# Kernel tuning notes

Hardware: AMD Instinct MI355X
Metric: run time of the kernel (lower is better)

Reference implementation:

```python
import jax, jax.numpy as jnp
import numpy as np

EPS = 1e-5
NUM_HEADS = 16


def activation_quant(x):
    # 8-bit activation quant with straight-through estimator
    scale = 127.0 / jnp.clip(jnp.max(jnp.abs(x), axis=-1, keepdims=True), 1e-5, None)
    y = jnp.clip(jnp.round(x * scale), -128.0, 127.0) / scale
    return x + jax.lax.stop_gradient(y - x)


def weight_quant(w):
    # ternary {-1,0,1} weight quant with STE
    scale = 1.0 / jnp.clip(jnp.mean(jnp.abs(w)), 1e-5, None)
    wq = jnp.clip(jnp.round(w * scale), -1.0, 1.0) / scale
    return w + jax.lax.stop_gradient(wq - w)


def bitlinear(x, w):
    # F.layer_norm(x, x.shape[1:]): normalize over ALL dims except batch, no affine
    axes = tuple(range(1, x.ndim))
    mu = jnp.mean(x, axis=axes, keepdims=True)
    var = jnp.var(x, axis=axes, keepdims=True)
    xn = (x - mu) * jax.lax.rsqrt(var + EPS)
    return jnp.einsum('bnd,od->bno', activation_quant(xn), weight_quant(w))


def layer_norm(x, gamma, beta):
    mu = jnp.mean(x, axis=-1, keepdims=True)
    var = jnp.var(x, axis=-1, keepdims=True)
    return (x - mu) * jax.lax.rsqrt(var + EPS) * gamma + beta


def setup_inputs() -> dict:
    key = jax.random.key(0)
    k0, k1, k2 = jax.random.split(key, 3)
    B, N, D = 2, 2048, 1024
    return {
        't': jnp.zeros((1,), jnp.float32),
        'x': jax.random.normal(k0, (B, N, D), jnp.float32),
        'w_qkv': jax.random.normal(k1, (3 * D, D), jnp.float32) * 0.02,
        'w_out': jax.random.normal(k2, (D, D), jnp.float32) * 0.02,
        'gamma': jnp.ones((D,), jnp.float32),
        'beta': jnp.zeros((D,), jnp.float32),
    }


def reference(t, x, w_qkv, w_out, gamma, beta):
    B, N, D = x.shape
    H = NUM_HEADS
    hd = D // H
    scale = hd ** -0.5
    h = layer_norm(x, gamma, beta)                     # [B,N,D]
    qkv = bitlinear(h, w_qkv).reshape(B, N, 3, H, hd)   # [B,N,3,H,hd]
    qkv = jnp.transpose(qkv, (2, 0, 3, 1, 4))           # [3,B,H,N,hd]
    q, k, v = qkv[0], qkv[1], qkv[2]
    attn = jax.nn.softmax(jnp.einsum('bhnd,bhmd->bhnm', q, k) * scale, axis=-1)
    out = jnp.einsum('bhnm,bhmd->bhnd', attn, v)        # [B,H,N,hd]
    out = jnp.transpose(out, (0, 2, 1, 3)).reshape(B, N, D)
    return bitlinear(out, w_out)
```

## Files before the change

### kernel.cpp

```cpp
#include <hip/hip_runtime.h>
#include <hip/hip_bf16.h>
#include <hip/hip_fp16.h>
#include <math.h>

typedef __hip_bfloat16 bf16;
typedef int   i32x4  __attribute__((ext_vector_type(4)));
typedef float f32x4  __attribute__((ext_vector_type(4)));
typedef float f32x16 __attribute__((ext_vector_type(16)));
typedef short bfx8   __attribute__((ext_vector_type(8)));

#define EPSV 1e-5f
#define NROWS 4096
#define DIM   1024
#define NSEQ  2048

__device__ __forceinline__ float fexp2(float x){ return __builtin_amdgcn_exp2f(x); }

__device__ __forceinline__ float ldv(const void* p, size_t i, int dt){
  if (dt == 0) return ((const float*)p)[i];
  if (dt == 1) return __bfloat162float(((const bf16*)p)[i]);
  return __half2float(((const __half*)p)[i]);
}
__device__ __forceinline__ float b2f(unsigned u){
  return __uint_as_float(u << 16);
}
__device__ __forceinline__ unsigned short f2bu(float f){
  bf16 t = __float2bfloat16(f);
  return *reinterpret_cast<unsigned short*>(&t);
}

__device__ __forceinline__ void detect(const void* c0, const void* c1,
                                       int& dt, const void*& g, const void*& bta){
  unsigned u0 = *(const unsigned*)c0;
  int gfirst = (u0 != 0u) ? 1 : 0;
  g   = gfirst ? c0 : c1;
  bta = gfirst ? c1 : c0;
  unsigned short g0 = *(const unsigned short*)g;
  dt = (g0 == 0x3F80) ? 1 : ((g0 == 0x3C00) ? 2 : 0);
}

__device__ __forceinline__ float blk_sum(float v, float* sm){
  #pragma unroll
  for (int o = 32; o > 0; o >>= 1) v += __shfl_xor(v, o, 64);
  __syncthreads();
  if ((threadIdx.x & 63) == 0) sm[threadIdx.x >> 6] = v;
  __syncthreads();
  return sm[0] + sm[1] + sm[2] + sm[3];
}
__device__ __forceinline__ double blk_sum_d(double v, double* sm){
  #pragma unroll
  for (int o = 32; o > 0; o >>= 1) v += __shfl_xor(v, o, 64);
  __syncthreads();
  if ((threadIdx.x & 63) == 0) sm[threadIdx.x >> 6] = v;
  __syncthreads();
  return sm[0] + sm[1] + sm[2] + sm[3];
}
__device__ __forceinline__ float blk_max(float v, float* sm){
  #pragma unroll
  for (int o = 32; o > 0; o >>= 1) v = fmaxf(v, __shfl_xor(v, o, 64));
  __syncthreads();
  if ((threadIdx.x & 63) == 0) sm[threadIdx.x >> 6] = v;
  __syncthreads();
  return fmaxf(fmaxf(sm[0], sm[1]), fmaxf(sm[2], sm[3]));
}

__global__ __launch_bounds__(256) void ln_rows(const void* __restrict__ x,
                                               const void* __restrict__ c0,
                                               const void* __restrict__ c1,
                                               unsigned short* __restrict__ h,
                                               double* __restrict__ lnp){
  __shared__ float sm[4];
  __shared__ double smd[4];
  int dt; const void *g, *bta;
  detect(c0, c1, dt, g, bta);
  int row = blockIdx.x;
  int tid = threadIdx.x;
  float v[4]; float s = 0.f;
  float gmv[4], btv[4];
  if (dt == 0){
    float4 v4 = ((const float4*)x)[(size_t)row*256 + tid];
    v[0]=v4.x; v[1]=v4.y; v[2]=v4.z; v[3]=v4.w;
    float4 gm4 = ((const float4*)g)[tid];
    float4 bt4 = ((const float4*)bta)[tid];
    gmv[0]=gm4.x; gmv[1]=gm4.y; gmv[2]=gm4.z; gmv[3]=gm4.w;
    btv[0]=bt4.x; btv[1]=bt4.y; btv[2]=bt4.z; btv[3]=bt4.w;
  } else {
    size_t base = (size_t)row * DIM;
    #pragma unroll
    for (int i = 0; i < 4; ++i){
      v[i]   = ldv(x, base + 4*tid + i, dt);
      gmv[i] = ldv(g, 4*tid + i, dt);
      btv[i] = ldv(bta, 4*tid + i, dt);
    }
  }
  #pragma unroll
  for (int i = 0; i < 4; ++i) s += v[i];
  s = blk_sum(s, sm);
  float mu = s * (1.f/1024.f);
  float d2 = 0.f;
  #pragma unroll
  for (int i = 0; i < 4; ++i){ float d = v[i] - mu; d2 += d*d; }
  d2 = blk_sum(d2, sm);
  float rs = rsqrtf(d2 * (1.f/1024.f) + EPSV);
  float hv[4];
  #pragma unroll
  for (int i = 0; i < 4; ++i) hv[i] = (v[i]-mu)*rs*gmv[i] + btv[i];
  unsigned p0 = (unsigned)f2bu(hv[0]) | ((unsigned)f2bu(hv[1]) << 16);
  unsigned p1 = (unsigned)f2bu(hv[2]) | ((unsigned)f2bu(hv[3]) << 16);
  ((uint2*)h)[(size_t)row*256 + tid] = make_uint2(p0, p1);
  double hs = 0.0, hq = 0.0;
  #pragma unroll
  for (int i = 0; i < 4; ++i){ hs += (double)hv[i]; hq += (double)hv[i]*(double)hv[i]; }
  hs = blk_sum_d(hs, smd);
  hq = blk_sum_d(hq, smd);
  if (tid == 0){ lnp[2*row] = hs; lnp[2*row + 1] = hq; }
}

__global__ __launch_bounds__(256) void abs_reduce_both(const void* __restrict__ wq,
                                                       const void* __restrict__ wo,
                                                       double* __restrict__ awp1,
                                                       double* __restrict__ awp2,
                                                       const void* __restrict__ c0,
                                                       const void* __restrict__ c1){
  __shared__ double smd[4];
  int dt; const void *g, *bta;
  detect(c0, c1, dt, g, bta);
  int blk = blockIdx.x;
  const void* w; int n; int nblk; int bi; double* part;
  if (blk < 512){ w = wq; n = 3*DIM*DIM; nblk = 512; bi = blk;      part = awp1; }
  else          { w = wo; n = DIM*DIM;   nblk = 128; bi = blk - 512; part = awp2; }
  double s = 0.0;
  if (dt == 0){
    const float4* w4 = (const float4*)w;
    int n4 = n >> 2;
    for (int i = bi*256 + threadIdx.x; i < n4; i += nblk*256){
      float4 v = w4[i];
      s += (double)(fabsf(v.x) + fabsf(v.y)) + (double)(fabsf(v.z) + fabsf(v.w));
    }
  } else {
    for (int i = bi*256 + threadIdx.x; i < n; i += nblk*256)
      s += (double)fabsf(ldv(w, i, dt));
  }
  s = blk_sum_d(s, smd);
  if (threadIdx.x == 0) part[bi] = s;
}

__global__ __launch_bounds__(256) void finalize1(float* acc,
                                                 const double* __restrict__ lnp,
                                                 const double* __restrict__ awp1,
                                                 const double* __restrict__ awp2){
  __shared__ double smd[4];
  int tid = threadIdx.x;
  double s0=0, q0=0, s1=0, q1=0, a1=0, a2=0;
  for (int i = tid; i < 2048; i += 256){
    s0 += lnp[2*i];          q0 += lnp[2*i + 1];
    s1 += lnp[2*(i+2048)];   q1 += lnp[2*(i+2048) + 1];
  }
  for (int i = tid; i < 512; i += 256) a1 += awp1[i];
  if (tid < 128) a2 = awp2[tid];
  s0 = blk_sum_d(s0, smd);  q0 = blk_sum_d(q0, smd);
  s1 = blk_sum_d(s1, smd);  q1 = blk_sum_d(q1, smd);
  a1 = blk_sum_d(a1, smd);  a2 = blk_sum_d(a2, smd);
  if (tid == 0){
    const double cnt = 2097152.0;
    double mu0 = s0/cnt, var0 = q0/cnt - mu0*mu0;
    double mu1 = s1/cnt, var1 = q1/cnt - mu1*mu1;
    acc[16] = (float)mu0; acc[17] = (float)(1.0 / sqrt(var0 + 1e-5));
    acc[18] = (float)mu1; acc[19] = (float)(1.0 / sqrt(var1 + 1e-5));
    acc[20] = (float)(1.0 / fmax(a1 / (3.0*1024.0*1024.0), 1e-5));
    acc[21] = (float)(1.0 / fmax(a2 / (1024.0*1024.0), 1e-5));
  }
}

__global__ __launch_bounds__(256) void finalize2(float* acc,
                                                 const double* __restrict__ atp){
  __shared__ double smd[4];
  int tid = threadIdx.x;
  double s0=0, q0=0, s1=0, q1=0;
  for (int i = tid; i < 512; i += 256){
    s0 += atp[2*i];          q0 += atp[2*i + 1];
    s1 += atp[2*(i+512)];    q1 += atp[2*(i+512) + 1];
  }
  s0 = blk_sum_d(s0, smd);  q0 = blk_sum_d(q0, smd);
  s1 = blk_sum_d(s1, smd);  q1 = blk_sum_d(q1, smd);
  if (tid == 0){
    const double cnt = 2097152.0;
    double mu0 = s0/cnt, var0 = q0/cnt - mu0*mu0;
    double mu1 = s1/cnt, var1 = q1/cnt - mu1*mu1;
    acc[22] = (float)mu0; acc[23] = (float)(1.0 / sqrt(var0 + 1e-5));
    acc[24] = (float)mu1; acc[25] = (float)(1.0 / sqrt(var1 + 1e-5));
  }
}

__global__ __launch_bounds__(256) void act_quant_i8b(const unsigned short* __restrict__ buf,
                                                     signed char* __restrict__ qout,
                                                     float* __restrict__ rscale,
                                                     const float* __restrict__ acc,
                                                     int statOff){
  __shared__ float sm[4];
  int row = blockIdx.x;
  int b = row >> 11;
  float mu = acc[statOff + 2*b], rs = acc[statOff + 2*b + 1];
  int tid = threadIdx.x;
  uint2 pk2 = ((const uint2*)buf)[(size_t)row*256 + tid];
  float v[4];
  v[0] = (b2f(pk2.x & 0xffffu) - mu) * rs;
  v[1] = (b2f(pk2.x >> 16)     - mu) * rs;
  v[2] = (b2f(pk2.y & 0xffffu) - mu) * rs;
  v[3] = (b2f(pk2.y >> 16)     - mu) * rs;
  float am = fmaxf(fmaxf(fabsf(v[0]), fabsf(v[1])), fmaxf(fabsf(v[2]), fabsf(v[3])));
  am = blk_max(am, sm);
  am = fmaxf(am, 1e-5f);
  float s127 = 127.f / am;
  unsigned pk = 0;
  #pragma unroll
  for (int i = 0; i < 4; ++i){
    float q = rintf(v[i] * s127);
    q = fminf(fmaxf(q, -128.f), 127.f);
    pk |= ((unsigned)(unsigned char)(signed char)q) << (8*i);
  }
  ((unsigned*)qout)[(size_t)row*256 + tid] = pk;
  if (tid == 0) rscale[row] = am * (1.f/127.f);
}

__global__ __launch_bounds__(256) void w_quant_both(const void* __restrict__ wqv,
                                                    const void* __restrict__ wov,
                                                    signed char* __restrict__ wqk,
                                                    signed char* __restrict__ wqo,
                                                    const float* __restrict__ acc,
                                                    const void* __restrict__ c0,
                                                    const void* __restrict__ c1){
  int dt; const void *g, *bta;
  detect(c0, c1, dt, g, bta);
  const int NQ4 = 786432;
  const int NT4 = 1048576;
  float s1 = acc[20], s2 = acc[21];
  if (dt == 0){
    for (int i = blockIdx.x*256 + threadIdx.x; i < NT4; i += gridDim.x*256){
      int inq = (i < NQ4);
      const float4* src = inq ? (const float4*)wqv : (const float4*)wov;
      unsigned* dst = inq ? (unsigned*)wqk : (unsigned*)wqo;
      int idx = inq ? i : (i - NQ4);
      float scale = inq ? s1 : s2;
      float4 v = src[idx];
      float vv[4] = {v.x, v.y, v.z, v.w};
      unsigned pk = 0;
      #pragma unroll
      for (int j = 0; j < 4; ++j){
        float q = rintf(vv[j] * scale);
        q = fminf(fmaxf(q, -1.f), 1.f);
        pk |= ((unsigned)(unsigned char)(signed char)q) << (8*j);
      }
      dst[idx] = pk;
    }
  } else {
    const int NQ = 3*DIM*DIM, NT = 4*DIM*DIM;
    for (int i = blockIdx.x*256 + threadIdx.x; i < NT; i += gridDim.x*256){
      int inq = (i < NQ);
      int idx = inq ? i : (i - NQ);
      float scale = inq ? s1 : s2;
      float q = rintf(ldv(inq ? wqv : wov, idx, dt) * scale);
      q = fminf(fmaxf(q, -1.f), 1.f);
      (inq ? wqk : wqo)[idx] = (signed char)q;
    }
  }
}

__global__ __launch_bounds__(256) void gemm_i8(const signed char* __restrict__ A,
                                               const signed char* __restrict__ W,
                                               const float* __restrict__ rscale,
                                               const float* __restrict__ acc, int sidx,
                                               float* __restrict__ Cf,
                                               bf16* __restrict__ Cb,
                                               int ldc, int writeBf, float q_prescale){
  __shared__ __attribute__((aligned(16))) signed char Asl[128][80];
  __shared__ __attribute__((aligned(16))) signed char Bsl[128][80];
  int tid = threadIdx.x, lane = tid & 63, w = tid >> 6;
  int wr = w >> 1, wc = w & 1;

  int nwgx = gridDim.x;
  int flat = blockIdx.y * nwgx + blockIdx.x;
  int nwg  = nwgx * gridDim.y;
  int cpx  = nwg >> 3;
  int swz  = (flat & 7) * cpx + (flat >> 3);
  int r0 = (swz / nwgx) * 128, o0 = (swz % nwgx) * 128;

  i32x4 zz = {0,0,0,0};
  i32x4 accv[4][4];
  #pragma unroll
  for (int m = 0; m < 4; ++m)
    #pragma unroll
    for (int n = 0; n < 4; ++n) accv[m][n] = zz;

  int sr0 = tid >> 2, sr1 = sr0 + 64;
  int sc  = (tid & 3) * 16;

  i32x4 a0, a1, b0, b1;
  a0 = *(const i32x4*)(A + (size_t)(r0 + sr0)*1024 + sc);
  a1 = *(const i32x4*)(A + (size_t)(r0 + sr1)*1024 + sc);
  b0 = *(const i32x4*)(W + (size_t)(o0 + sr0)*1024 + sc);
  b1 = *(const i32x4*)(W + (size_t)(o0 + sr1)*1024 + sc);

  for (int k0 = 0; k0 < 1024; k0 += 64){
    __syncthreads();
    *(i32x4*)&Asl[sr0][sc] = a0;
    *(i32x4*)&Asl[sr1][sc] = a1;
    *(i32x4*)&Bsl[sr0][sc] = b0;
    *(i32x4*)&Bsl[sr1][sc] = b1;
    __syncthreads();
    if (k0 + 64 < 1024){
      int kn = k0 + 64;
      a0 = *(const i32x4*)(A + (size_t)(r0 + sr0)*1024 + kn + sc);
      a1 = *(const i32x4*)(A + (size_t)(r0 + sr1)*1024 + kn + sc);
      b0 = *(const i32x4*)(W + (size_t)(o0 + sr0)*1024 + kn + sc);
      b1 = *(const i32x4*)(W + (size_t)(o0 + sr1)*1024 + kn + sc);
    }
    i32x4 af[4], bfr[4];
    #pragma unroll
    for (int m = 0; m < 4; ++m)
      af[m] = *(const i32x4*)&Asl[wr*64 + m*16 + (lane & 15)][(lane >> 4) * 16];
    #pragma unroll
    for (int n = 0; n < 4; ++n)
      bfr[n] = *(const i32x4*)&Bsl[wc*64 + n*16 + (lane & 15)][(lane >> 4) * 16];
    __builtin_amdgcn_s_setprio(1);
    #pragma unroll
    for (int m = 0; m < 4; ++m)
      #pragma unroll
      for (int n = 0; n < 4; ++n)
        accv[m][n] = __builtin_amdgcn_mfma_i32_16x16x64_i8(af[m], bfr[n], accv[m][n], 0, 0, 0);
    __builtin_amdgcn_s_setprio(0);
  }

  float wsc = acc[sidx];
  float cs = (o0 < 1024) ? q_prescale : 1.0f;
  float rf[4][4];
  #pragma unroll
  for (int m = 0; m < 4; ++m)
    #pragma unroll
    for (int r = 0; r < 4; ++r)
      rf[m][r] = rscale[r0 + wr*64 + m*16 + ((lane >> 4) << 2) + r] / wsc * cs;

  #pragma unroll
  for (int m = 0; m < 4; ++m)
    #pragma unroll
    for (int n = 0; n < 4; ++n)
      #pragma unroll
      for (int r = 0; r < 4; ++r){
        float val = (float)accv[m][n][r] * rf[m][r];
        size_t row = (size_t)(r0 + wr*64 + m*16 + ((lane >> 4) << 2) + r);
        int col = o0 + wc*64 + n*16 + (lane & 15);
        if (writeBf) Cb[row * ldc + col] = __float2bfloat16(val);
        else         Cf[row * ldc + col] = val;
      }
}

__global__ __launch_bounds__(128) void attn_mfma(const bf16* __restrict__ qkv,
                                                 unsigned short* __restrict__ out,
                                                 double* __restrict__ atp){
  __shared__ __attribute__((aligned(16))) unsigned short K_lds[64][64];
  __shared__ __attribute__((aligned(16))) unsigned short Vt_lds[64][64];
  __shared__ double smd[2];

  int tid = threadIdx.x, lane = tid & 63, w = tid >> 6;
  int l31 = lane & 31, hi = lane >> 5;

  int flat = blockIdx.y * 32 + blockIdx.x;
  int slot = flat & 7, idx = flat >> 3;
  int bh = slot * 4 + (idx >> 5);
  int qx = idx & 31;
  int b = bh >> 4, h = bh & 15;
  int n0 = qx * 64;
  const unsigned short* qg = (const unsigned short*)qkv;

  char* kB = (char*)K_lds;
  char* vB = (char*)Vt_lds;

  int qrow = b*NSEQ + n0 + w*32 + l31;
  bfx8 qf[4];
  #pragma unroll
  for (int kk = 0; kk < 4; ++kk)
    qf[kk] = *(const bfx8*)(qg + (size_t)qrow*3072 + h*64 + kk*16 + hi*8);

  float m_run = -INFINITY, l_run = 0.f;
  f32x16 acco[2];
  #pragma unroll
  for (int n = 0; n < 2; ++n)
    #pragma unroll
    for (int r = 0; r < 16; ++r) acco[n][r] = 0.f;

  int krow = tid & 63;
  int r2 = tid & 31, dw = tid >> 5;
  int k7 = krow & 7;
  int q7 = l31 & 7;

  bfx8 kc[4], vv[4];
  auto LOADT = [&](int kt){
    size_t kvb = (size_t)(b*NSEQ + kt*64);
    #pragma unroll
    for (int j = 0; j < 4; ++j)
      kc[j] = *(const bfx8*)(qg + (kvb + krow)*3072 + 1024 + h*64 + (w + 2*j)*8);
    vv[0] = *(const bfx8*)(qg + (kvb + 2*r2    )*3072 + 2048 + h*64 + dw*8);
    vv[1] = *(const bfx8*)(qg + (kvb + 2*r2 + 1)*3072 + 2048 + h*64 + dw*8);
    vv[2] = *(const bfx8*)(qg + (kvb + 2*r2    )*3072 + 2048 + h*64 + (dw+4)*8);
    vv[3] = *(const bfx8*)(qg + (kvb + 2*r2 + 1)*3072 + 2048 + h*64 + (dw+4)*8);
  };
  LOADT(0);

  for (int kt = 0; kt < NSEQ/64; ++kt){
    __syncthreads();
    #pragma unroll
    for (int j = 0; j < 4; ++j)
      *(bfx8*)(kB + krow*128 + (((w + 2*j) ^ k7) << 4)) = kc[j];
    #pragma unroll
    for (int u = 0; u < 8; ++u){
      unsigned w0 = (unsigned)(unsigned short)vv[0][u] |
                    ((unsigned)(unsigned short)vv[1][u] << 16);
      unsigned w1 = (unsigned)(unsigned short)vv[2][u] |
                    ((unsigned)(unsigned short)vv[3][u] << 16);
      *(unsigned*)(vB + (dw*8 + u)*128     + ((4*r2) ^ (u << 4))) = w0;
      *(unsigned*)(vB + ((dw+4)*8 + u)*128 + ((4*r2) ^ (u << 4))) = w1;
    }
    __syncthreads();
    if (kt + 1 < NSEQ/64) LOADT(kt + 1);

    f32x16 s0, s1;
    #pragma unroll
    for (int r = 0; r < 16; ++r){ s0[r] = 0.f; s1[r] = 0.f; }
    #pragma unroll
    for (int kk = 0; kk < 4; ++kk){
      bfx8 kb0 = *(const bfx8*)(kB + l31*128        + (((2*kk + hi) ^ q7) << 4));
      bfx8 kb1 = *(const bfx8*)(kB + (32 + l31)*128 + (((2*kk + hi) ^ q7) << 4));
      __builtin_amdgcn_s_setprio(1);
      s0 = __builtin_amdgcn_mfma_f32_32x32x16_bf16(kb0, qf[kk], s0, 0, 0, 0);
      s1 = __builtin_amdgcn_mfma_f32_32x32x16_bf16(kb1, qf[kk], s1, 0, 0, 0);
      __builtin_amdgcn_s_setprio(0);
    }

    float pa0 = fmaxf(s0[0], s0[1]),  pa1 = fmaxf(s0[2], s0[3]);
    float pa2 = fmaxf(s0[4], s0[5]),  pa3 = fmaxf(s0[6], s0[7]);
    #pragma unroll
    for (int r = 8; r < 16; r += 4){
      pa0 = fmaxf(pa0, fmaxf(s0[r], s0[r+1]));
      pa1 = fmaxf(pa1, fmaxf(s0[r+2], s0[r+3]));
    }
    #pragma unroll
    for (int r = 0; r < 16; r += 4){
      pa2 = fmaxf(pa2, fmaxf(s1[r], s1[r+1]));
      pa3 = fmaxf(pa3, fmaxf(s1[r+2], s1[r+3]));
    }
    float pm = fmaxf(fmaxf(pa0, pa1), fmaxf(pa2, pa3));
    pm = fmaxf(pm, __shfl_xor(pm, 32, 64));
    if (__any(pm > m_run + 11.5415605f)){
      float mnew = fmaxf(m_run, pm);
      float corr = fexp2(m_run - mnew);
      m_run = mnew;
      l_run *= corr;
      #pragma unroll
      for (int r = 0; r < 16; ++r){
        float ca = __shfl(corr, (r & 3) + 8*(r >> 2) + 4*hi, 64);
        acco[0][r] *= ca; acco[1][r] *= ca;
      }
    }
    float ts = 0.f;
    #pragma unroll
    for (int r = 0; r < 16; ++r){
      s0[r] = fexp2(s0[r] - m_run); ts += s0[r];
      s1[r] = fexp2(s1[r] - m_run); ts += s1[r];
    }
    ts += __shfl_xor(ts, 32, 64);
    l_run += ts;

    #pragma unroll
    for (int kvb2 = 0; kvb2 < 2; ++kvb2){
      const f32x16& s = kvb2 ? s1 : s0;
      #pragma unroll
      for (int kk2 = 0; kk2 < 2; ++kk2){
        int bse = kk2 * 8;
        unsigned wa, wb2, wc, wd;
        asm("v_cvt_pk_bf16_f32 %0, %1, %2" : "=v"(wa)  : "v"(s[bse+0]), "v"(s[bse+1]));
        asm("v_cvt_pk_bf16_f32 %0, %1, %2" : "=v"(wb2) : "v"(s[bse+4]), "v"(s[bse+5]));
        asm("v_cvt_pk_bf16_f32 %0, %1, %2" : "=v"(wc)  : "v"(s[bse+2]), "v"(s[bse+3]));
        asm("v_cvt_pk_bf16_f32 %0, %1, %2" : "=v"(wd)  : "v"(s[bse+6]), "v"(s[bse+7]));
        asm("v_permlane32_swap_b32 %0, %1" : "+v"(wa), "+v"(wb2));
        asm("v_permlane32_swap_b32 %0, %1" : "+v"(wc), "+v"(wd));
        unsigned pw[4] = {wa, wc, wb2, wd};
        bfx8 pfr = *(bfx8*)pw;
        #pragma unroll
        for (int n = 0; n < 2; ++n){
          bfx8 vb = *(const bfx8*)(vB + (n*32 + l31)*128 +
                                   (((kvb2*4 + kk2*2 + hi) ^ q7) << 4));
          __builtin_amdgcn_s_setprio(1);
          acco[n] = __builtin_amdgcn_mfma_f32_32x32x16_bf16(pfr, vb, acco[n], 0, 0, 0);
          __builtin_amdgcn_s_setprio(0);
        }
      }
    }
  }

  float il = 1.f / l_run;
  float ila[16];
  #pragma unroll
  for (int r = 0; r < 16; ++r)
    ila[r] = __shfl(il, (r & 3) + 8*(r >> 2) + 4*hi, 64);
  double ssum = 0.0, ssq = 0.0;
  #pragma unroll
  for (int n = 0; n < 2; ++n)
    #pragma unroll
    for (int r = 0; r < 16; ++r){
      float o = acco[n][r] * ila[r];
      int orow = b*NSEQ + n0 + w*32 + (r & 3) + 8*(r >> 2) + 4*hi;
      out[(size_t)orow * DIM + h*64 + n*32 + l31] = f2bu(o);
      ssum += (double)o; ssq += (double)o * (double)o;
    }
  #pragma unroll
  for (int o = 32; o > 0; o >>= 1){ ssum += __shfl_xor(ssum, o, 64); ssq += __shfl_xor(ssq, o, 64); }
  __syncthreads();
  if (lane == 0){ smd[w] = ssum; }
  __syncthreads();
  double tsum = smd[0] + smd[1];
  __syncthreads();
  if (lane == 0){ smd[w] = ssq; }
  __syncthreads();
  double tsq = smd[0] + smd[1];
  if (tid == 0){
    int bflat = bh * 32 + qx;
    atp[2*bflat] = tsum; atp[2*bflat + 1] = tsq;
  }
}

extern "C" void kernel_launch(void* const* d_in, const int* in_sizes, int n_in,
                              void* d_out, int out_size, void* d_ws, size_t ws_size,
                              hipStream_t stream) {
  int ix = -1, iwq = -1, iwo = -1, ig0 = -1, ig1 = -1;
  for (int i = 0; i < n_in; ++i){
    int s = in_sizes[i];
    if      (s == 4194304) ix  = i;
    else if (s == 3145728) iwq = i;
    else if (s == 1048576) iwo = i;
    else if (s == 1024){ if (ig0 < 0) ig0 = i; else ig1 = i; }
  }
  if (ix < 0 || iwq < 0 || iwo < 0 || ig0 < 0 || ig1 < 0){ ix=1; iwq=2; iwo=3; ig0=4; ig1=5; }
  const void* x     = d_in[ix];
  const void* w_qkv = d_in[iwq];
  const void* w_out = d_in[iwo];
  const void* g0    = d_in[ig0];
  const void* g1    = d_in[ig1];

  char* ws = (char*)d_ws;
  float*  acc     = (float*)ws;
  float*  rscale1 = (float*)(ws + 12288);
  float*  rscale2 = (float*)(ws + 28672);
  double* lnp     = (double*)(ws + 65536);
  double* awp1    = (double*)(ws + 131072);
  double* awp2    = (double*)(ws + 135168);
  double* atp     = (double*)(ws + 139264);
  unsigned short* h    = (unsigned short*)(ws + (1u<<20));
  signed char*  h_i8   = (signed char*)(ws + (17u<<20));
  signed char*  wqk_i8 = (signed char*)(ws + (21u<<20));
  signed char*  wqo_i8 = (signed char*)(ws + (24u<<20));
  bf16*         qkvb   = (bf16*)       (ws + (25u<<20));
  signed char*  a2_i8  = (signed char*)(ws + (49u<<20));
  unsigned short* aout = h;

  ln_rows<<<NROWS, 256, 0, stream>>>(x, g0, g1, h, lnp);
  abs_reduce_both<<<640, 256, 0, stream>>>(w_qkv, w_out, awp1, awp2, g0, g1);
  finalize1<<<1, 256, 0, stream>>>(acc, lnp, awp1, awp2);
  act_quant_i8b<<<NROWS, 256, 0, stream>>>(h, h_i8, rscale1, acc, 16);
  w_quant_both<<<1024, 256, 0, stream>>>(w_qkv, w_out, wqk_i8, wqo_i8, acc, g0, g1);
  gemm_i8<<<dim3(24, 32), 256, 0, stream>>>(h_i8, wqk_i8, rscale1, acc, 20,
                                            nullptr, qkvb, 3072, 1, 0.125f * 1.44269504f);
  attn_mfma<<<dim3(32, 32), 128, 0, stream>>>(qkvb, aout, atp);
  finalize2<<<1, 256, 0, stream>>>(acc, atp);
  act_quant_i8b<<<NROWS, 256, 0, stream>>>(aout, a2_i8, rscale2, acc, 22);
  gemm_i8<<<dim3(8, 32), 256, 0, stream>>>(a2_i8, wqo_i8, rscale2, acc, 21,
                                           (float*)d_out, nullptr, 1024, 0, 1.0f);
}
```

Baseline: 151.0 us.

## Split attention KV range across two wave pairs and merge partial softmax

The attention kernel now runs 256 threads per block, with two wave pairs each handling half of the key/value sequence in separate LDS buffers. The two partial outputs are merged through shared memory using the running max and sum. The per-block sum and sum-of-squares reduction moves out into a new attn_stats kernel that rereads the bf16 output. This doubles the waves working per query tile to shorten the serial KV loop and raise occupancy, at the cost of an extra kernel launch, an extra read of the output, and LDS merge traffic.

```diff
diff --git a/kernel.cpp b/kernel.cpp
--- a/kernel.cpp
+++ b/kernel.cpp
@@ -354,15 +354,15 @@
       }
 }
 
-__global__ __launch_bounds__(128) void attn_mfma(const bf16* __restrict__ qkv,
-                                                 unsigned short* __restrict__ out,
-                                                 double* __restrict__ atp){
-  __shared__ __attribute__((aligned(16))) unsigned short K_lds[64][64];
-  __shared__ __attribute__((aligned(16))) unsigned short Vt_lds[64][64];
-  __shared__ double smd[2];
+__global__ __launch_bounds__(256, 4) void attn_mfma(const bf16* __restrict__ qkv,
+                                                    unsigned short* __restrict__ out){
+  __shared__ __attribute__((aligned(16))) unsigned short K_lds[2][64][64];
+  __shared__ __attribute__((aligned(16))) unsigned short Vt_lds[2][64][64];
 
   int tid = threadIdx.x, lane = tid & 63, w = tid >> 6;
+  int p = w >> 1, wq = w & 1;
   int l31 = lane & 31, hi = lane >> 5;
+  int ptid = tid & 127;
 
   int flat = blockIdx.y * 32 + blockIdx.x;
   int slot = flat & 7, idx = flat >> 3;
@@ -372,10 +372,10 @@
   int n0 = qx * 64;
   const unsigned short* qg = (const unsigned short*)qkv;
 
-  char* kB = (char*)K_lds;
-  char* vB = (char*)Vt_lds;
-
-  int qrow = b*NSEQ + n0 + w*32 + l31;
+  char* kB = (char*)K_lds + p*8192;
+  char* vB = (char*)Vt_lds + p*8192;
+
+  int qrow = b*NSEQ + n0 + wq*32 + l31;
   bfx8 qf[4];
   #pragma unroll
   for (int kk = 0; kk < 4; ++kk)
@@ -388,17 +388,18 @@
     #pragma unroll
     for (int r = 0; r < 16; ++r) acco[n][r] = 0.f;
 
-  int krow = tid & 63;
-  int r2 = tid & 31, dw = tid >> 5;
+  int krow = ptid & 63;
+  int r2 = ptid & 31, dw = ptid >> 5;
+  int wp = ptid >> 6;
   int k7 = krow & 7;
   int q7 = l31 & 7;
 
   bfx8 kc[4], vv[4];
   auto LOADT = [&](int kt){
-    size_t kvb = (size_t)(b*NSEQ + kt*64);
+    size_t kvb = (size_t)(b*NSEQ + p*1024 + kt*64);
     #pragma unroll
     for (int j = 0; j < 4; ++j)
-      kc[j] = *(const bfx8*)(qg + (kvb + krow)*3072 + 1024 + h*64 + (w + 2*j)*8);
+      kc[j] = *(const bfx8*)(qg + (kvb + krow)*3072 + 1024 + h*64 + (wp + 2*j)*8);
     vv[0] = *(const bfx8*)(qg + (kvb + 2*r2    )*3072 + 2048 + h*64 + dw*8);
     vv[1] = *(const bfx8*)(qg + (kvb + 2*r2 + 1)*3072 + 2048 + h*64 + dw*8);
     vv[2] = *(const bfx8*)(qg + (kvb + 2*r2    )*3072 + 2048 + h*64 + (dw+4)*8);
@@ -406,11 +407,11 @@
   };
   LOADT(0);
 
-  for (int kt = 0; kt < NSEQ/64; ++kt){
+  for (int kt = 0; kt < 16; ++kt){
     __syncthreads();
     #pragma unroll
     for (int j = 0; j < 4; ++j)
-      *(bfx8*)(kB + krow*128 + (((w + 2*j) ^ k7) << 4)) = kc[j];
+      *(bfx8*)(kB + krow*128 + (((wp + 2*j) ^ k7) << 4)) = kc[j];
     #pragma unroll
     for (int u = 0; u < 8; ++u){
       unsigned w0 = (unsigned)(unsigned short)vv[0][u] |
@@ -421,7 +422,7 @@
       *(unsigned*)(vB + ((dw+4)*8 + u)*128 + ((4*r2) ^ (u << 4))) = w1;
     }
     __syncthreads();
-    if (kt + 1 < NSEQ/64) LOADT(kt + 1);
+    if (kt + 1 < 16) LOADT(kt + 1);
 
     f32x16 s0, s1;
     #pragma unroll
@@ -497,35 +498,61 @@
     }
   }
 
-  float il = 1.f / l_run;
-  float ila[16];
-  #pragma unroll
-  for (int r = 0; r < 16; ++r)
-    ila[r] = __shfl(il, (r & 3) + 8*(r >> 2) + 4*hi, 64);
+  __syncthreads();
+  float*  Om  = (float*)K_lds;
+  float2* mlL = (float2*)Vt_lds;
+  if (p == 1){
+    #pragma unroll
+    for (int n = 0; n < 2; ++n)
+      #pragma unroll
+      for (int r = 0; r < 16; ++r){
+        int row = wq*32 + (r & 3) + 8*(r >> 2) + 4*hi;
+        Om[row*64 + n*32 + l31] = acco[n][r];
+      }
+    if (hi == 0) mlL[wq*32 + l31] = make_float2(m_run, l_run);
+  }
+  __syncthreads();
+  if (p == 0){
+    float2 ml1 = mlL[wq*32 + l31];
+    float m  = fmaxf(m_run, ml1.x);
+    float c0 = fexp2(m_run - m), c1 = fexp2(ml1.x - m);
+    float inv = 1.f / (l_run*c0 + ml1.y*c1);
+    float f0l = c0*inv, f1l = c1*inv;
+    float f0[16], f1[16];
+    #pragma unroll
+    for (int r = 0; r < 16; ++r){
+      int rl = (r & 3) + 8*(r >> 2) + 4*hi;
+      f0[r] = __shfl(f0l, rl, 64);
+      f1[r] = __shfl(f1l, rl, 64);
+    }
+    #pragma unroll
+    for (int n = 0; n < 2; ++n)
+      #pragma unroll
+      for (int r = 0; r < 16; ++r){
+        int row = wq*32 + (r & 3) + 8*(r >> 2) + 4*hi;
+        float o = acco[n][r]*f0[r] + Om[row*64 + n*32 + l31]*f1[r];
+        out[(size_t)(b*NSEQ + n0 + row) * DIM + h*64 + n*32 + l31] = f2bu(o);
+      }
+  }
+}
+
+__global__ __launch_bounds__(256) void attn_stats(const unsigned short* __restrict__ out,
+                                                  double* __restrict__ atp){
+  __shared__ double smd[4];
+  int tid = threadIdx.x;
+  size_t base4 = (size_t)blockIdx.x * 1024;
   double ssum = 0.0, ssq = 0.0;
   #pragma unroll
-  for (int n = 0; n < 2; ++n)
-    #pragma unroll
-    for (int r = 0; r < 16; ++r){
-      float o = acco[n][r] * ila[r];
-      int orow = b*NSEQ + n0 + w*32 + (r & 3) + 8*(r >> 2) + 4*hi;
-      out[(size_t)orow * DIM + h*64 + n*32 + l31] = f2bu(o);
-      ssum += (double)o; ssq += (double)o * (double)o;
-    }
-  #pragma unroll
-  for (int o = 32; o > 0; o >>= 1){ ssum += __shfl_xor(ssum, o, 64); ssq += __shfl_xor(ssq, o, 64); }
-  __syncthreads();
-  if (lane == 0){ smd[w] = ssum; }
-  __syncthreads();
-  double tsum = smd[0] + smd[1];
-  __syncthreads();
-  if (lane == 0){ smd[w] = ssq; }
-  __syncthreads();
-  double tsq = smd[0] + smd[1];
-  if (tid == 0){
-    int bflat = bh * 32 + qx;
-    atp[2*bflat] = tsum; atp[2*bflat + 1] = tsq;
-  }
+  for (int j = 0; j < 4; ++j){
+    uint2 pk = ((const uint2*)out)[base4 + tid + j*256];
+    float v0 = b2f(pk.x & 0xffffu), v1 = b2f(pk.x >> 16);
+    float v2 = b2f(pk.y & 0xffffu), v3 = b2f(pk.y >> 16);
+    ssum += (double)v0 + (double)v1 + (double)v2 + (double)v3;
+    ssq  += (double)v0*v0 + (double)v1*v1 + (double)v2*v2 + (double)v3*v3;
+  }
+  ssum = blk_sum_d(ssum, smd);
+  ssq  = blk_sum_d(ssq, smd);
+  if (tid == 0){ atp[2*blockIdx.x] = ssum; atp[2*blockIdx.x + 1] = ssq; }
 }
 
 extern "C" void kernel_launch(void* const* d_in, const int* in_sizes, int n_in,
@@ -569,7 +596,8 @@
   w_quant_both<<<1024, 256, 0, stream>>>(w_qkv, w_out, wqk_i8, wqo_i8, acc, g0, g1);
   gemm_i8<<<dim3(24, 32), 256, 0, stream>>>(h_i8, wqk_i8, rscale1, acc, 20,
                                             nullptr, qkvb, 3072, 1, 0.125f * 1.44269504f);
-  attn_mfma<<<dim3(32, 32), 128, 0, stream>>>(qkvb, aout, atp);
+  attn_mfma<<<dim3(32, 32), 256, 0, stream>>>(qkvb, aout);
+  attn_stats<<<1024, 256, 0, stream>>>(aout, atp);
   finalize2<<<1, 256, 0, stream>>>(acc, atp);
   act_quant_i8b<<<NROWS, 256, 0, stream>>>(aout, a2_i8, rscale2, acc, 22);
   gemm_i8<<<dim3(8, 32), 256, 0, stream>>>(a2_i8, wqo_i8, rscale2, acc, 21,
```

Result: slower. 275.9 us (+82.8%).

## Double-buffer K/V tiles in LDS to cut a barrier per iteration

Applied to the files above, without the earlier changes.

The attention kernel now keeps two LDS buffers for the K and transposed V tiles. Each iteration writes the next tile into the alternate buffer while computing on the current one, and global prefetch runs two tiles ahead. This leaves one __syncthreads per iteration instead of two and overlaps LDS writes with MFMA work. LDS use doubles to 32KB per block, which may reduce occupancy, and register pressure rises from holding the prefetched tile longer.

```diff
diff --git a/kernel.cpp b/kernel.cpp
--- a/kernel.cpp
+++ b/kernel.cpp
@@ -357,8 +357,8 @@
 __global__ __launch_bounds__(128) void attn_mfma(const bf16* __restrict__ qkv,
                                                  unsigned short* __restrict__ out,
                                                  double* __restrict__ atp){
-  __shared__ __attribute__((aligned(16))) unsigned short K_lds[64][64];
-  __shared__ __attribute__((aligned(16))) unsigned short Vt_lds[64][64];
+  __shared__ __attribute__((aligned(16))) unsigned short K_lds[2][64][64];
+  __shared__ __attribute__((aligned(16))) unsigned short Vt_lds[2][64][64];
   __shared__ double smd[2];
 
   int tid = threadIdx.x, lane = tid & 63, w = tid >> 6;
@@ -404,32 +404,42 @@
     vv[2] = *(const bfx8*)(qg + (kvb + 2*r2    )*3072 + 2048 + h*64 + (dw+4)*8);
     vv[3] = *(const bfx8*)(qg + (kvb + 2*r2 + 1)*3072 + 2048 + h*64 + (dw+4)*8);
   };
-  LOADT(0);
-
-  for (int kt = 0; kt < NSEQ/64; ++kt){
-    __syncthreads();
+  auto WRITET = [&](int buf){
+    int bo = buf * 8192;
     #pragma unroll
     for (int j = 0; j < 4; ++j)
-      *(bfx8*)(kB + krow*128 + (((w + 2*j) ^ k7) << 4)) = kc[j];
+      *(bfx8*)(kB + bo + krow*128 + (((w + 2*j) ^ k7) << 4)) = kc[j];
     #pragma unroll
     for (int u = 0; u < 8; ++u){
       unsigned w0 = (unsigned)(unsigned short)vv[0][u] |
                     ((unsigned)(unsigned short)vv[1][u] << 16);
       unsigned w1 = (unsigned)(unsigned short)vv[2][u] |
                     ((unsigned)(unsigned short)vv[3][u] << 16);
-      *(unsigned*)(vB + (dw*8 + u)*128     + ((4*r2) ^ (u << 4))) = w0;
-      *(unsigned*)(vB + ((dw+4)*8 + u)*128 + ((4*r2) ^ (u << 4))) = w1;
-    }
-    __syncthreads();
-    if (kt + 1 < NSEQ/64) LOADT(kt + 1);
+      *(unsigned*)(vB + bo + (dw*8 + u)*128     + ((4*r2) ^ (u << 4))) = w0;
+      *(unsigned*)(vB + bo + ((dw+4)*8 + u)*128 + ((4*r2) ^ (u << 4))) = w1;
+    }
+  };
+
+  LOADT(0);
+  WRITET(0);
+  __syncthreads();
+  LOADT(1);
+
+  int cur = 0;
+  for (int kt = 0; kt < NSEQ/64; ++kt){
+    if (kt + 1 < NSEQ/64){
+      WRITET(cur ^ 1);
+      if (kt + 2 < NSEQ/64) LOADT(kt + 2);
+    }
+    int bo = cur * 8192;
 
     f32x16 s0, s1;
     #pragma unroll
     for (int r = 0; r < 16; ++r){ s0[r] = 0.f; s1[r] = 0.f; }
     #pragma unroll
     for (int kk = 0; kk < 4; ++kk){
-      bfx8 kb0 = *(const bfx8*)(kB + l31*128        + (((2*kk + hi) ^ q7) << 4));
-      bfx8 kb1 = *(const bfx8*)(kB + (32 + l31)*128 + (((2*kk + hi) ^ q7) << 4));
+      bfx8 kb0 = *(const bfx8*)(kB + bo + l31*128        + (((2*kk + hi) ^ q7) << 4));
+      bfx8 kb1 = *(const bfx8*)(kB + bo + (32 + l31)*128 + (((2*kk + hi) ^ q7) << 4));
       __builtin_amdgcn_s_setprio(1);
       s0 = __builtin_amdgcn_mfma_f32_32x32x16_bf16(kb0, qf[kk], s0, 0, 0, 0);
       s1 = __builtin_amdgcn_mfma_f32_32x32x16_bf16(kb1, qf[kk], s1, 0, 0, 0);
@@ -487,7 +497,7 @@
         bfx8 pfr = *(bfx8*)pw;
         #pragma unroll
         for (int n = 0; n < 2; ++n){
-          bfx8 vb = *(const bfx8*)(vB + (n*32 + l31)*128 +
+          bfx8 vb = *(const bfx8*)(vB + bo + (n*32 + l31)*128 +
                                    (((kvb2*4 + kk2*2 + hi) ^ q7) << 4));
           __builtin_amdgcn_s_setprio(1);
           acco[n] = __builtin_amdgcn_mfma_f32_32x32x16_bf16(pfr, vb, acco[n], 0, 0, 0);
@@ -495,6 +505,9 @@
         }
       }
     }
+
+    __syncthreads();
+    cur ^= 1;
   }
 
   float il = 1.f / l_run;
@@ -513,13 +526,16 @@
       ssum += (double)o; ssq += (double)o * (double)o;
     }
   #pragma unroll
-  for (int o = 32; o > 0; o >>= 1){ ssum += __shfl_xor(ssum, o, 64); ssq += __shfl_xor(ssq, o, 64); }
-  __syncthreads();
-  if (lane == 0){ smd[w] = ssum; }
+  for (int o2 = 32; o2 > 0; o2 >>= 1){
+    ssum += __shfl_xor(ssum, o2, 64);
+    ssq  += __shfl_xor(ssq,  o2, 64);
+  }
+  __syncthreads();
+  if (lane == 0) smd[w] = ssum;
   __syncthreads();
   double tsum = smd[0] + smd[1];
   __syncthreads();
-  if (lane == 0){ smd[w] = ssq; }
+  if (lane == 0) smd[w] = ssq;
   __syncthreads();
   double tsq = smd[0] + smd[1];
   if (tid == 0){
```

Result: no change. 151.9 us (+0.6%).
